# Kernel tuning notes

Hardware: AMD Instinct MI355X
Metric: run time of the kernel (lower is better)

Reference implementation:

```python
import jax, jax.numpy as jnp
import numpy as np

N = 8192      # sequence length (rows of query/key/value)
D = 768       # model dim (Conv1d in_channels)
DFF = 2048    # FFN hidden dim (Conv1d out_channels)


def setup_inputs() -> dict:
    key = jax.random.key(0)
    ks = jax.random.split(key, 7)
    query = jax.random.normal(ks[0], (N, D), dtype=jnp.float32)
    k = jax.random.normal(ks[1], (N, D), dtype=jnp.float32)
    value = jax.random.normal(ks[2], (N, D), dtype=jnp.float32)
    # Conv1d(kernel_size=1) == dense layer: weight [out,in], bias [out]
    W1 = jax.random.normal(ks[3], (DFF, D), dtype=jnp.float32) * 0.02
    b1 = jax.random.normal(ks[4], (DFF,), dtype=jnp.float32) * 0.02
    W2 = jax.random.normal(ks[5], (D, DFF), dtype=jnp.float32) * 0.02
    b2 = jax.random.normal(ks[6], (D,), dtype=jnp.float32) * 0.02
    return {"query": query, "key": k, "value": value,
            "W1": W1, "b1": b1, "W2": W2, "b2": b2}


def reference(query, key, value, W1, b1, W2, b2):
    # manual attention: no 1/sqrt(d) scaling in the original module
    scores = jnp.matmul(query, key.T)              # [N, N]
    attn = jax.nn.softmax(scores, axis=-1)         # [N, N]
    context = jnp.matmul(attn, value)              # [N, D]
    # conv1x1 -> ReLU -> conv1x1 (2-layer MLP)
    h = jax.nn.relu(jnp.matmul(context, W1.T) + b1)  # [N, DFF]
    out = jnp.matmul(h, W2.T) + b2                   # [N, D]
    return out
```

## Files before the change

kernel.cpp:

```cpp
#include <hip/hip_runtime.h>
#include <cstdint>
#include <cstddef>

#define DEV __device__ __forceinline__

typedef _Float16 f16;
typedef __attribute__((ext_vector_type(8))) _Float16 f16x8;
typedef __attribute__((ext_vector_type(4))) float f32x4;

DEV unsigned short f2h(float f) {
  f16 h = (f16)f;
  return __builtin_bit_cast(unsigned short, h);
}

DEV void async_ld16(const void* g, void* l) {
  __builtin_amdgcn_global_load_lds(
      (__attribute__((address_space(1))) unsigned int*)(uintptr_t)g,
      (__attribute__((address_space(3))) unsigned int*)(uint32_t)(uintptr_t)l,
      16, 0, 0);
}

#define MFMA16(d, a, b_) (d) = __builtin_amdgcn_mfma_f32_16x16x32_f16((a), (b_), (d), 0, 0, 0)

template <int BN, int EPI, bool RELU, bool HASBIAS, bool ALPHA, bool XCD>
__global__ __launch_bounds__(512, 2) void gemm256(
    const unsigned short* __restrict__ A, const unsigned short* __restrict__ B,
    void* __restrict__ Cp, const float* __restrict__ bias,
    const unsigned short* __restrict__ alp, int Mtot,
    int K, int lda, int ldb, int ldc, int nt, int mt, int sl) {
  extern __shared__ char smem[];
  constexpr int FN = BN / 64;
  constexpr int WCW = BN / 4;
  constexpr int BUFSZ = 32768 + BN * 128;
  const int NT = K >> 6;

  int mb, nb, zb;
  {
    const int b = blockIdx.x;
    if (XCD) {
      const int xcd = b & 7, q = b >> 3;
      nb = q % nt;
      const int rest = q / nt;
      zb = rest % sl;
      mb = xcd * (mt >> 3) + rest / sl;
    } else {
      nb = b % nt;
      const int t = b / nt;
      mb = t % mt;
      zb = t / mt;
    }
  }
  const int bm = mb << 8, bn = nb * BN;
  const unsigned koff = (unsigned)zb * (unsigned)K;

  const int tid = threadIdx.x;
  const int wave = tid >> 6, lane = tid & 63;
  const int wr = wave >> 2, wc = wave & 3;
  const int mr = lane & 15, quad = lane >> 4;

  const int slot = tid & 7, rr = tid >> 3;
  const int ce = (slot ^ (rr & 7)) << 3;

  f32x4 acc[8][FN] = {};
  f16x8 av0[4][2], av1[4][2], bv0[2][2], bv1[FN - 2][2];
  const f16* alb = (const f16*)(smem + 2 * BUFSZ);

  if (ALPHA) {
    const int ntl = K >> 7;
    const unsigned short* g0 = alp + (size_t)(zb * ntl) * Mtot + bm;
    uint4* s = (uint4*)(smem + 2 * BUFSZ);
    const int nu4 = (ntl << 5);
    for (int idx = tid; idx < nu4; idx += 512) {
      const int tt = idx >> 5;
      const int ru = (idx & 31) << 3;
      s[idx] = *(const uint4*)(g0 + (size_t)tt * Mtot + ru);
    }
  }

  auto stA = [&](int h, int Ts) {
    const int t_ = Ts >= NT ? Ts - NT : Ts;
    const unsigned kk = koff + (unsigned)(t_ << 6);
    char* l = smem + (Ts & 1) * BUFSZ + h * 16384 + wave * 1024;
#pragma unroll
    for (int p = 0; p < 2; ++p) {
      const unsigned off = (unsigned)(bm + p * 128 + h * 64 + rr) * (unsigned)lda + kk + ce;
      async_ld16(A + off, l + p * 8192);
    }
  };
  auto stB = [&](int h, int Ts) {
    const int t_ = Ts >= NT ? Ts - NT : Ts;
    const unsigned kk = koff + (unsigned)(t_ << 6);
    char* l = smem + (Ts & 1) * BUFSZ + 32768 + h * 16384 + wave * 1024;
    if (BN == 256) {
#pragma unroll
      for (int p = 0; p < 2; ++p) {
        const int g = bn + p * 128 + (rr >> 5) * 64 + h * 32 + (rr & 31);
        async_ld16(B + ((unsigned)g * (unsigned)ldb + kk + ce), l + p * 8192);
      }
    } else if (h == 0) {
#pragma unroll
      for (int p = 0; p < 2; ++p) {
        const int g = bn + (p * 2 + (rr >> 5)) * 48 + (rr & 31);
        async_ld16(B + ((unsigned)g * (unsigned)ldb + kk + ce), l + p * 8192);
      }
    } else {
      const int g = bn + (rr >> 4) * 48 + 32 + (rr & 15);
      async_ld16(B + ((unsigned)g * (unsigned)ldb + kk + ce), l);
    }
  };
  auto rdA = [&](int bufc, int i, int ks) {
    const int r = wr * 64 + (i & 3) * 16 + mr;
    return *(const f16x8*)(smem + bufc + (i >> 2) * 16384 + r * 128 +
                           ((((ks << 2) | quad) ^ (mr & 7)) << 4));
  };
  auto rdB0 = [&](int bufc, int j, int ks) {
    const int rb = wc * 32 + j * 16 + mr;
    return *(const f16x8*)(smem + bufc + 32768 + rb * 128 +
                           ((((ks << 2) | quad) ^ (mr & 7)) << 4));
  };
  auto rdB1 = [&](int bufc, int j, int ks) {
    const int rb = (BN == 256) ? (wc * 32 + (j - 2) * 16 + mr) : (wc * 16 + mr);
    return *(const f16x8*)(smem + bufc + 32768 + 16384 + rb * 128 +
                           ((((ks << 2) | quad) ^ (mr & 7)) << 4));
  };

  stA(0, 0); stB(0, 0); stA(1, 0); stB(1, 0);
  stA(0, 1); stB(0, 1); stA(1, 1);
  if (ALPHA) asm volatile("s_waitcnt lgkmcnt(0)" ::: "memory");
  asm volatile("s_waitcnt vmcnt(6)" ::: "memory");
  __builtin_amdgcn_s_barrier();

  for (int T = 0; T < NT; ++T) {
    const int bufc = (T & 1) * BUFSZ;
    f16 a0_[4], a1_[4];
#pragma unroll
    for (int i = 0; i < 4; ++i) { av0[i][0] = rdA(bufc, i, 0); av0[i][1] = rdA(bufc, i, 1); }
    if (ALPHA) {
#pragma unroll
      for (int i = 0; i < 4; ++i) a0_[i] = alb[(T >> 1) * 256 + wr * 128 + i * 16 + mr];
    }
    stB(1, T + 1);
    __builtin_amdgcn_s_barrier();
    asm volatile("s_waitcnt lgkmcnt(0)" ::: "memory");
    __builtin_amdgcn_sched_barrier(0);
    if (ALPHA) {
#pragma unroll
      for (int i = 0; i < 4; ++i) { av0[i][0] = av0[i][0] * a0_[i]; av0[i][1] = av0[i][1] * a0_[i]; }
    }
    if (T) {
      __builtin_amdgcn_s_setprio(1);
#pragma unroll
      for (int i = 0; i < 4; ++i)
#pragma unroll
        for (int j = 0; j < FN - 2; ++j) {
          MFMA16(acc[4 + i][2 + j], av1[i][0], bv1[j][0]);
          MFMA16(acc[4 + i][2 + j], av1[i][1], bv1[j][1]);
        }
      __builtin_amdgcn_s_setprio(0);
    }
    __builtin_amdgcn_s_barrier();
#pragma unroll
    for (int j = 0; j < 2; ++j) { bv0[j][0] = rdB0(bufc, j, 0); bv0[j][1] = rdB0(bufc, j, 1); }
    stA(0, T + 2);
    __builtin_amdgcn_s_barrier();
    asm volatile("s_waitcnt lgkmcnt(0)" ::: "memory");
    __builtin_amdgcn_sched_barrier(0);
    __builtin_amdgcn_s_setprio(1);
#pragma unroll
    for (int i = 0; i < 4; ++i)
#pragma unroll
      for (int j = 0; j < 2; ++j) {
        MFMA16(acc[i][j], av0[i][0], bv0[j][0]);
        MFMA16(acc[i][j], av0[i][1], bv0[j][1]);
      }
    __builtin_amdgcn_s_setprio(0);
    __builtin_amdgcn_s_barrier();
#pragma unroll
    for (int i = 0; i < 4; ++i) { av1[i][0] = rdA(bufc, 4 + i, 0); av1[i][1] = rdA(bufc, 4 + i, 1); }
    if (ALPHA) {
#pragma unroll
      for (int i = 0; i < 4; ++i) a1_[i] = alb[(T >> 1) * 256 + wr * 128 + 64 + i * 16 + mr];
    }
    stB(0, T + 2);
    __builtin_amdgcn_s_barrier();
    asm volatile("s_waitcnt lgkmcnt(0)" ::: "memory");
    __builtin_amdgcn_sched_barrier(0);
    if (ALPHA) {
#pragma unroll
      for (int i = 0; i < 4; ++i) { av1[i][0] = av1[i][0] * a1_[i]; av1[i][1] = av1[i][1] * a1_[i]; }
    }
    __builtin_amdgcn_s_setprio(1);
#pragma unroll
    for (int i = 0; i < 4; ++i)
#pragma unroll
      for (int j = 0; j < 2; ++j) {
        MFMA16(acc[4 + i][j], av1[i][0], bv0[j][0]);
        MFMA16(acc[4 + i][j], av1[i][1], bv0[j][1]);
      }
    __builtin_amdgcn_s_setprio(0);
    __builtin_amdgcn_s_barrier();
#pragma unroll
    for (int j = 0; j < FN - 2; ++j) { bv1[j][0] = rdB1(bufc, 2 + j, 0); bv1[j][1] = rdB1(bufc, 2 + j, 1); }
    stA(1, T + 2);
    __builtin_amdgcn_s_barrier();
    asm volatile("s_waitcnt lgkmcnt(0)" ::: "memory");
    __builtin_amdgcn_sched_barrier(0);
    __builtin_amdgcn_s_setprio(1);
#pragma unroll
    for (int i = 0; i < 4; ++i)
#pragma unroll
      for (int j = 0; j < FN - 2; ++j) {
        MFMA16(acc[i][2 + j], av0[i][0], bv1[j][0]);
        MFMA16(acc[i][2 + j], av0[i][1], bv1[j][1]);
      }
    __builtin_amdgcn_s_setprio(0);
    asm volatile("s_waitcnt vmcnt(6)" ::: "memory");
    __builtin_amdgcn_s_barrier();
  }
  __builtin_amdgcn_s_setprio(1);
#pragma unroll
  for (int i = 0; i < 4; ++i)
#pragma unroll
    for (int j = 0; j < FN - 2; ++j) {
      MFMA16(acc[4 + i][2 + j], av1[i][0], bv1[j][0]);
      MFMA16(acc[4 + i][2 + j], av1[i][1], bv1[j][1]);
    }
  __builtin_amdgcn_s_setprio(0);
  asm volatile("s_waitcnt vmcnt(0)" ::: "memory");
  __builtin_amdgcn_s_barrier();

#pragma unroll
  for (int i = 0; i < 8; ++i) {
#pragma unroll
    for (int j = 0; j < FN; ++j) {
      const int col = bn + wc * WCW + j * 16 + mr;
      float bb = 0.f;
      if (HASBIAS) bb = bias[col];
#pragma unroll
      for (int r = 0; r < 4; ++r) {
        const int row = bm + wr * 128 + i * 16 + quad * 4 + r;
        float v = acc[i][j][r];
        if (HASBIAS) v += bb;
        if (RELU) v = fmaxf(v, 0.f);
        if (EPI == 2)
          atomicAdd(&((float*)Cp)[(size_t)row * ldc + col], v);
        else
          ((unsigned short*)Cp)[(size_t)row * ldc + col] = f2h(v);
      }
    }
  }
}

__global__ __launch_bounds__(512, 2) void qk256(
    const unsigned short* __restrict__ A, const unsigned short* __restrict__ B,
    unsigned short* __restrict__ P, float* __restrict__ stm,
    float* __restrict__ stl, int M, int K, int lda, int ldb, int ldc) {
  extern __shared__ char smem[];
  const int NT = K >> 6;

  const int b = blockIdx.x;
  const int xcd = b & 7, c = b >> 3;
  const int mb = ((c >> 5) << 3) | ((c >> 2) & 7);
  const int nb = (xcd << 2) | (c & 3);
  const int bm = mb << 8, bn = nb << 8;

  const int tid = threadIdx.x;
  const int wave = tid >> 6, lane = tid & 63;
  const int wr = wave >> 2, wc = wave & 3;
  const int mr = lane & 15, quad = lane >> 4;

  const int slot = tid & 7, rr = tid >> 3;
  const int ce = (slot ^ (rr & 7)) << 3;

  f32x4 acc[8][4] = {};
  f16x8 av0[4][2], av1[4][2], bv0[2][2], bv1[2][2];

  auto stA = [&](int h, int Ts) {
    const int t = Ts >= NT ? Ts - NT : Ts;
    const int kk = t << 6;
    char* l = smem + ((Ts & 1) << 16) + h * 16384 + wave * 1024;
#pragma unroll
    for (int p = 0; p < 2; ++p) {
      const unsigned off = (unsigned)(bm + p * 128 + h * 64 + rr) * (unsigned)lda + kk + ce;
      async_ld16(A + off, l + p * 8192);
    }
  };
  auto stB = [&](int h, int Ts) {
    const int t = Ts >= NT ? Ts - NT : Ts;
    const int kk = t << 6;
    char* l = smem + ((Ts & 1) << 16) + 32768 + h * 16384 + wave * 1024;
#pragma unroll
    for (int p = 0; p < 2; ++p) {
      const unsigned off =
          (unsigned)(bn + p * 128 + (rr >> 5) * 64 + h * 32 + (rr & 31)) * (unsigned)ldb + kk + ce;
      async_ld16(B + off, l + p * 8192);
    }
  };
  auto rdA = [&](int bufc, int i, int ks) {
    const int r = wr * 64 + (i & 3) * 16 + mr;
    return *(const f16x8*)(smem + bufc + (i >> 2) * 16384 + r * 128 +
                           ((((ks << 2) | quad) ^ (mr & 7)) << 4));
  };
  auto rdB = [&](int bufc, int j, int ks) {
    const int r = wc * 32 + (j & 1) * 16 + mr;
    return *(const f16x8*)(smem + bufc + 32768 + (j >> 1) * 16384 + r * 128 +
                           ((((ks << 2) | quad) ^ (mr & 7)) << 4));
  };

  stA(0, 0); stB(0, 0); stA(1, 0); stB(1, 0);
  stA(0, 1); stB(0, 1); stA(1, 1);
  asm volatile("s_waitcnt vmcnt(6)" ::: "memory");
  __builtin_amdgcn_s_barrier();

  for (int T = 0; T < NT; ++T) {
    const int bufc = (T & 1) << 16;
#pragma unroll
    for (int i = 0; i < 4; ++i) { av0[i][0] = rdA(bufc, i, 0); av0[i][1] = rdA(bufc, i, 1); }
    stB(1, T + 1);
    __builtin_amdgcn_s_barrier();
    asm volatile("s_waitcnt lgkmcnt(0)" ::: "memory");
    __builtin_amdgcn_sched_barrier(0);
    if (T) {
      __builtin_amdgcn_s_setprio(1);
#pragma unroll
      for (int i = 0; i < 4; ++i)
#pragma unroll
        for (int j = 0; j < 2; ++j) {
          MFMA16(acc[4 + i][2 + j], av1[i][0], bv1[j][0]);
          MFMA16(acc[4 + i][2 + j], av1[i][1], bv1[j][1]);
        }
      __builtin_amdgcn_s_setprio(0);
    }
    __builtin_amdgcn_s_barrier();
#pragma unroll
    for (int j = 0; j < 2; ++j) { bv0[j][0] = rdB(bufc, j, 0); bv0[j][1] = rdB(bufc, j, 1); }
    stA(0, T + 2);
    __builtin_amdgcn_s_barrier();
    asm volatile("s_waitcnt lgkmcnt(0)" ::: "memory");
    __builtin_amdgcn_sched_barrier(0);
    __builtin_amdgcn_s_setprio(1);
#pragma unroll
    for (int i = 0; i < 4; ++i)
#pragma unroll
      for (int j = 0; j < 2; ++j) {
        MFMA16(acc[i][j], av0[i][0], bv0[j][0]);
        MFMA16(acc[i][j], av0[i][1], bv0[j][1]);
      }
    __builtin_amdgcn_s_setprio(0);
    __builtin_amdgcn_s_barrier();
#pragma unroll
    for (int i = 0; i < 4; ++i) { av1[i][0] = rdA(bufc, 4 + i, 0); av1[i][1] = rdA(bufc, 4 + i, 1); }
    stB(0, T + 2);
    __builtin_amdgcn_s_barrier();
    asm volatile("s_waitcnt lgkmcnt(0)" ::: "memory");
    __builtin_amdgcn_sched_barrier(0);
    __builtin_amdgcn_s_setprio(1);
#pragma unroll
    for (int i = 0; i < 4; ++i)
#pragma unroll
      for (int j = 0; j < 2; ++j) {
        MFMA16(acc[4 + i][j], av1[i][0], bv0[j][0]);
        MFMA16(acc[4 + i][j], av1[i][1], bv0[j][1]);
      }
    __builtin_amdgcn_s_setprio(0);
    __builtin_amdgcn_s_barrier();
#pragma unroll
    for (int j = 0; j < 2; ++j) { bv1[j][0] = rdB(bufc, 2 + j, 0); bv1[j][1] = rdB(bufc, 2 + j, 1); }
    stA(1, T + 2);
    __builtin_amdgcn_s_barrier();
    asm volatile("s_waitcnt lgkmcnt(0)" ::: "memory");
    __builtin_amdgcn_sched_barrier(0);
    __builtin_amdgcn_s_setprio(1);
#pragma unroll
    for (int i = 0; i < 4; ++i)
#pragma unroll
      for (int j = 0; j < 2; ++j) {
        MFMA16(acc[i][2 + j], av0[i][0], bv1[j][0]);
        MFMA16(acc[i][2 + j], av0[i][1], bv1[j][1]);
      }
    __builtin_amdgcn_s_setprio(0);
    asm volatile("s_waitcnt vmcnt(6)" ::: "memory");
    __builtin_amdgcn_s_barrier();
  }
  __builtin_amdgcn_s_setprio(1);
#pragma unroll
  for (int i = 0; i < 4; ++i)
#pragma unroll
    for (int j = 0; j < 2; ++j) {
      MFMA16(acc[4 + i][2 + j], av1[i][0], bv1[j][0]);
      MFMA16(acc[4 + i][2 + j], av1[i][1], bv1[j][1]);
    }
  __builtin_amdgcn_s_setprio(0);
  asm volatile("s_waitcnt vmcnt(0)" ::: "memory");
  __builtin_amdgcn_s_barrier();

  float* sred = (float*)smem;
  float* ssum = (float*)(smem + 4096);
  const int hc = wc >> 1;
  float Mh[8][4];

#pragma unroll
  for (int i = 0; i < 8; ++i)
#pragma unroll
    for (int r = 0; r < 4; ++r) {
      float m = acc[i][0][r];
#pragma unroll
      for (int j = 1; j < 4; ++j) m = fmaxf(m, acc[i][j][r]);
      m = fmaxf(m, __shfl_xor(m, 1));
      m = fmaxf(m, __shfl_xor(m, 2));
      m = fmaxf(m, __shfl_xor(m, 4));
      m = fmaxf(m, __shfl_xor(m, 8));
      if (mr == 0) sred[(wr * 128 + i * 16 + quad * 4 + r) * 4 + wc] = m;
    }
  __syncthreads();
#pragma unroll
  for (int i = 0; i < 8; ++i)
#pragma unroll
    for (int r = 0; r < 4; ++r) {
      const int row_l = wr * 128 + i * 16 + quad * 4 + r;
      Mh[i][r] = fmaxf(sred[row_l * 4 + 2 * hc], sred[row_l * 4 + 2 * hc + 1]);
    }
#pragma unroll
  for (int i = 0; i < 8; ++i)
#pragma unroll
    for (int r = 0; r < 4; ++r) {
      const int row_l = wr * 128 + i * 16 + quad * 4 + r;
      float l = 0.f;
#pragma unroll
      for (int j = 0; j < 4; ++j) {
        const float e = __expf(acc[i][j][r] - Mh[i][r]);
        P[(size_t)(bm + row_l) * ldc + (bn + wc * 64 + j * 16 + mr)] = f2h(e);
        l += e;
      }
      l += __shfl_xor(l, 1);
      l += __shfl_xor(l, 2);
      l += __shfl_xor(l, 4);
      l += __shfl_xor(l, 8);
      if (mr == 0) ssum[row_l * 4 + wc] = l;
    }
  __syncthreads();
  if ((wc & 1) == 0 && mr == 0) {
#pragma unroll
    for (int i = 0; i < 8; ++i)
#pragma unroll
      for (int r = 0; r < 4; ++r) {
        const int row_l = wr * 128 + i * 16 + quad * 4 + r;
        const int tile = nb * 2 + hc;
        stm[(size_t)tile * M + bm + row_l] = Mh[i][r];
        stl[(size_t)tile * M + bm + row_l] =
            ssum[row_l * 4 + 2 * hc] + ssum[row_l * 4 + 2 * hc + 1];
      }
  }
}

__global__ __launch_bounds__(256) void combine_alpha(
    const float* __restrict__ stm, const float* __restrict__ stl,
    unsigned short* __restrict__ alp, int ntile, int Mtot) {
  const int row = blockIdx.x * 4 + (threadIdx.x >> 6);
  const int t = threadIdx.x & 63;
  float m = (t < ntile) ? stm[(size_t)t * Mtot + row] : -1e30f;
  float M = m;
#pragma unroll
  for (int o = 1; o < 64; o <<= 1) M = fmaxf(M, __shfl_xor(M, o));
  float l = (t < ntile) ? stl[(size_t)t * Mtot + row] : 0.f;
  float c = l * __expf(m - M);
#pragma unroll
  for (int o = 1; o < 64; o <<= 1) c += __shfl_xor(c, o);
  if (t < ntile) alp[(size_t)t * Mtot + row] = f2h(__expf(m - M) / c);
}

__global__ __launch_bounds__(256) void cvt_f16(const float* __restrict__ in,
                                               unsigned short* __restrict__ out, int n) {
  int i = blockIdx.x * 256 + threadIdx.x;
  if (i < n) out[i] = f2h(in[i]);
}

__global__ __launch_bounds__(256) void bias_fill(float* __restrict__ out,
                                                 const float* __restrict__ b, int d) {
  int i = blockIdx.x * 256 + threadIdx.x;
  out[i] = b[i % d];
}

__global__ __launch_bounds__(256) void vt_kernel(const float* __restrict__ V,
                                                 unsigned short* __restrict__ vT) {
  __shared__ float t[32][33];
  const int bx = blockIdx.x, by = blockIdx.y;
  const int x = threadIdx.x, y = threadIdx.y;
#pragma unroll
  for (int r = 0; r < 4; ++r)
    t[y + r * 8][x] = V[(size_t)(by * 32 + y + r * 8) * 768 + bx * 32 + x];
  __syncthreads();
#pragma unroll
  for (int r = 0; r < 4; ++r)
    vT[(size_t)(bx * 32 + y + r * 8) * 8192 + by * 32 + x] = f2h(t[x][y + r * 8]);
}

extern "C" void kernel_launch(void* const* d_in, const int* in_sizes, int n_in,
                              void* d_out, int out_size, void* d_ws, size_t ws_size,
                              hipStream_t stream) {
  const int N = 8192, D = 768, DFF = 2048;
  const float* Q  = (const float*)d_in[0];
  const float* Km = (const float*)d_in[1];
  const float* V  = (const float*)d_in[2];
  const float* W1 = (const float*)d_in[3];
  const float* b1 = (const float*)d_in[4];
  const float* W2 = (const float*)d_in[5];
  const float* b2 = (const float*)d_in[6];

  char* w = (char*)d_ws;
  size_t off = 0;
  auto take = [&](size_t bytes) { void* p = w + off; off += bytes; return p; };
  unsigned short* qh   = (unsigned short*)take((size_t)N * D * 2);
  unsigned short* kh   = (unsigned short*)take((size_t)N * D * 2);
  unsigned short* vT   = (unsigned short*)take((size_t)N * D * 2);
  unsigned short* ctx16= (unsigned short*)take((size_t)N * D * 2);
  float*          ctx32= (float*)take((size_t)N * D * 4);
  unsigned short* hb   = (unsigned short*)take((size_t)N * DFF * 2);
  unsigned short* w1h  = (unsigned short*)take((size_t)DFF * D * 2);
  unsigned short* w2h  = (unsigned short*)take((size_t)D * DFF * 2);
  float*          stm  = (float*)take((size_t)64 * N * 4);
  float*          stl  = (float*)take((size_t)64 * N * 4);
  unsigned short* alp  = (unsigned short*)take((size_t)64 * N * 2);
  unsigned short* Pp   = (unsigned short*)take((size_t)N * N * 2);
  (void)ws_size;

  cvt_f16<<<(N * D) / 256, 256, 0, stream>>>(Q, qh, N * D);
  cvt_f16<<<(N * D) / 256, 256, 0, stream>>>(Km, kh, N * D);
  vt_kernel<<<dim3(D / 32, N / 32), dim3(32, 8), 0, stream>>>(V, vT);
  cvt_f16<<<(DFF * D) / 256, 256, 0, stream>>>(W1, w1h, DFF * D);
  cvt_f16<<<(D * DFF) / 256, 256, 0, stream>>>(W2, w2h, D * DFF);
  hipMemsetAsync(ctx32, 0, (size_t)N * D * 4, stream);
  bias_fill<<<(N * D) / 256, 256, 0, stream>>>((float*)d_out, b2, D);

  {
    hipFuncSetAttribute((const void*)qk256,
                        hipFuncAttributeMaxDynamicSharedMemorySize, 131072);
    qk256<<<(N / 256) * (N / 256), 512, 131072, stream>>>(
        qh, kh, Pp, stm, stl, N, D, D, D, N);
  }
  combine_alpha<<<N / 4, 256, 0, stream>>>(stm, stl, alp, 64, N);

  {
    const int nt = D / 192, mt = N / 256, sl = 2;
    constexpr int BUFSZ = 32768 + 192 * 128;
    const int smem_sz = 2 * BUFSZ + ((N / 2) >> 7) * 256 * 2;
    hipFuncSetAttribute((const void*)gemm256<192, 2, false, false, true, true>,
                        hipFuncAttributeMaxDynamicSharedMemorySize, smem_sz);
    gemm256<192, 2, false, false, true, true><<<nt * mt * sl, 512, smem_sz, stream>>>(
        Pp, vT, ctx32, nullptr, alp, N,
        N / sl, N, N, D, nt, mt, sl);
  }
  cvt_f16<<<(N * D) / 256, 256, 0, stream>>>(ctx32, ctx16, N * D);

  {
    const int nt = DFF / 256, mt = N / 256;
    hipFuncSetAttribute((const void*)gemm256<256, 0, true, true, false, true>,
                        hipFuncAttributeMaxDynamicSharedMemorySize, 131072);
    gemm256<256, 0, true, true, false, true><<<nt * mt, 512, 131072, stream>>>(
        ctx16, w1h, hb, b1, nullptr, N,
        D, D, D, DFF, nt, mt, 1);
  }
  {
    const int nt = D / 192, mt = N / 256, sl = 2;
    constexpr int BUFSZ = 32768 + 192 * 128;
    hipFuncSetAttribute((const void*)gemm256<192, 2, false, false, false, true>,
                        hipFuncAttributeMaxDynamicSharedMemorySize, 2 * BUFSZ);
    gemm256<192, 2, false, false, false, true><<<nt * mt * sl, 512, 2 * BUFSZ, stream>>>(
        hb, w2h, (float*)d_out, nullptr, nullptr, N,
        DFF / sl, DFF, DFF, D, nt, mt, sl);
  }
}
```

Baseline: 552.4 us.

## Replace split-K atomics with per-slice stores and fused combine kernels

Both split-K GEMMs (P·V and the second FFN layer) now store each K-slice's partial result to its own fp32 buffer instead of atomically adding into a zeroed or bias-prefilled output. Small combine kernels then add the two slices, one also converting to fp16 and the other adding the bias. This removes the memset and the bias_fill pass. The four separate fp32-to-fp16 conversion launches are merged into one vectorized prep kernel. The cost is extra scratch traffic: the slices reuse the hb region and the P buffer, so correctness depends on those buffers being free at that point.

Measured after the change: 480.6 us. 13.0% less time.

```diff
diff --git a/kernel.cpp b/kernel.cpp
--- a/kernel.cpp
+++ b/kernel.cpp
@@ -7,6 +7,7 @@
 typedef _Float16 f16;
 typedef __attribute__((ext_vector_type(8))) _Float16 f16x8;
 typedef __attribute__((ext_vector_type(4))) float f32x4;
+typedef __attribute__((ext_vector_type(4))) unsigned short us4;
 
 DEV unsigned short f2h(float f) {
   f16 h = (f16)f;
@@ -244,6 +245,8 @@
         if (RELU) v = fmaxf(v, 0.f);
         if (EPI == 2)
           atomicAdd(&((float*)Cp)[(size_t)row * ldc + col], v);
+        else if (EPI == 1)
+          ((float*)Cp)[(size_t)zb * Mtot * ldc + (size_t)row * ldc + col] = v;
         else
           ((unsigned short*)Cp)[(size_t)row * ldc + col] = f2h(v);
       }
@@ -469,16 +472,54 @@
   if (t < ntile) alp[(size_t)t * Mtot + row] = f2h(__expf(m - M) / c);
 }
 
-__global__ __launch_bounds__(256) void cvt_f16(const float* __restrict__ in,
-                                               unsigned short* __restrict__ out, int n) {
+__global__ __launch_bounds__(256) void prep4(
+    const float* __restrict__ Q, const float* __restrict__ Km,
+    const float* __restrict__ W1, const float* __restrict__ W2,
+    unsigned short* __restrict__ qh, unsigned short* __restrict__ kh,
+    unsigned short* __restrict__ w1h, unsigned short* __restrict__ w2h,
+    int nqk4, int nw4) {
   int i = blockIdx.x * 256 + threadIdx.x;
-  if (i < n) out[i] = f2h(in[i]);
-}
-
-__global__ __launch_bounds__(256) void bias_fill(float* __restrict__ out,
-                                                 const float* __restrict__ b, int d) {
+  if (i >= 2 * nqk4 + 2 * nw4) return;
+  const float* src;
+  unsigned short* dst;
+  int j = i;
+  if (j < nqk4) { src = Q; dst = qh; }
+  else if ((j -= nqk4) < nqk4) { src = Km; dst = kh; }
+  else if ((j -= nqk4) < nw4) { src = W1; dst = w1h; }
+  else { j -= nw4; src = W2; dst = w2h; }
+  f32x4 v = ((const f32x4*)src)[j];
+  us4 r;
+#pragma unroll
+  for (int k = 0; k < 4; ++k) r[k] = f2h(v[k]);
+  ((us4*)dst)[j] = r;
+}
+
+__global__ __launch_bounds__(256) void combine2_cvt(const f32x4* __restrict__ a,
+                                                    const f32x4* __restrict__ b,
+                                                    us4* __restrict__ o, int n4) {
   int i = blockIdx.x * 256 + threadIdx.x;
-  out[i] = b[i % d];
+  if (i < n4) {
+    f32x4 va = a[i], vb = b[i];
+    us4 r;
+#pragma unroll
+    for (int j = 0; j < 4; ++j) r[j] = f2h(va[j] + vb[j]);
+    o[i] = r;
+  }
+}
+
+__global__ __launch_bounds__(256) void combine2_bias(const f32x4* __restrict__ a,
+                                                     const f32x4* __restrict__ b,
+                                                     const float* __restrict__ bias,
+                                                     f32x4* __restrict__ o, int n4, int d4) {
+  int i = blockIdx.x * 256 + threadIdx.x;
+  if (i < n4) {
+    f32x4 va = a[i], vb = b[i];
+    const int c = (i % d4) * 4;
+    f32x4 r;
+#pragma unroll
+    for (int j = 0; j < 4; ++j) r[j] = va[j] + vb[j] + bias[c + j];
+    o[i] = r;
+  }
 }
 
 __global__ __launch_bounds__(256) void vt_kernel(const float* __restrict__ V,
@@ -522,15 +563,13 @@
   float*          stl  = (float*)take((size_t)64 * N * 4);
   unsigned short* alp  = (unsigned short*)take((size_t)64 * N * 2);
   unsigned short* Pp   = (unsigned short*)take((size_t)N * N * 2);
+  float* ctxsh = ctx32;
+  float* osh   = (float*)Pp;
   (void)ws_size;
 
-  cvt_f16<<<(N * D) / 256, 256, 0, stream>>>(Q, qh, N * D);
-  cvt_f16<<<(N * D) / 256, 256, 0, stream>>>(Km, kh, N * D);
+  prep4<<<((2 * N * D + 2 * DFF * D) / 4 + 255) / 256, 256, 0, stream>>>(
+      Q, Km, W1, W2, qh, kh, w1h, w2h, N * D / 4, DFF * D / 4);
   vt_kernel<<<dim3(D / 32, N / 32), dim3(32, 8), 0, stream>>>(V, vT);
-  cvt_f16<<<(DFF * D) / 256, 256, 0, stream>>>(W1, w1h, DFF * D);
-  cvt_f16<<<(D * DFF) / 256, 256, 0, stream>>>(W2, w2h, D * DFF);
-  hipMemsetAsync(ctx32, 0, (size_t)N * D * 4, stream);
-  bias_fill<<<(N * D) / 256, 256, 0, stream>>>((float*)d_out, b2, D);
 
   {
     hipFuncSetAttribute((const void*)qk256,
@@ -544,13 +583,14 @@
     const int nt = D / 192, mt = N / 256, sl = 2;
     constexpr int BUFSZ = 32768 + 192 * 128;
     const int smem_sz = 2 * BUFSZ + ((N / 2) >> 7) * 256 * 2;
-    hipFuncSetAttribute((const void*)gemm256<192, 2, false, false, true, true>,
+    hipFuncSetAttribute((const void*)gemm256<192, 1, false, false, true, true>,
                         hipFuncAttributeMaxDynamicSharedMemorySize, smem_sz);
-    gemm256<192, 2, false, false, true, true><<<nt * mt * sl, 512, smem_sz, stream>>>(
-        Pp, vT, ctx32, nullptr, alp, N,
+    gemm256<192, 1, false, false, true, true><<<nt * mt * sl, 512, smem_sz, stream>>>(
+        Pp, vT, ctxsh, nullptr, alp, N,
         N / sl, N, N, D, nt, mt, sl);
   }
-  cvt_f16<<<(N * D) / 256, 256, 0, stream>>>(ctx32, ctx16, N * D);
+  combine2_cvt<<<(N * D / 4 + 255) / 256, 256, 0, stream>>>(
+      (const f32x4*)ctxsh, (const f32x4*)(ctxsh + (size_t)N * D), (us4*)ctx16, N * D / 4);
 
   {
     const int nt = DFF / 256, mt = N / 256;
@@ -563,10 +603,13 @@
   {
     const int nt = D / 192, mt = N / 256, sl = 2;
     constexpr int BUFSZ = 32768 + 192 * 128;
-    hipFuncSetAttribute((const void*)gemm256<192, 2, false, false, false, true>,
+    hipFuncSetAttribute((const void*)gemm256<192, 1, false, false, false, true>,
                         hipFuncAttributeMaxDynamicSharedMemorySize, 2 * BUFSZ);
-    gemm256<192, 2, false, false, false, true><<<nt * mt * sl, 512, 2 * BUFSZ, stream>>>(
-        hb, w2h, (float*)d_out, nullptr, nullptr, N,
+    gemm256<192, 1, false, false, false, true><<<nt * mt * sl, 512, 2 * BUFSZ, stream>>>(
+        hb, w2h, osh, nullptr, nullptr, N,
         DFF / sl, DFF, DFF, D, nt, mt, sl);
   }
-}
+  combine2_bias<<<(N * D / 4 + 255) / 256, 256, 0, stream>>>(
+      (const f32x4*)osh, (const f32x4*)(osh + (size_t)N * D), b2,
+      (f32x4*)d_out, N * D / 4, D / 4);
+}
```
